# Optimization experiments

Hardware: AMD Instinct MI355X
Metric: run time of the kernel (lower is better)

The kernel has to match this reference:

```python
import jax, jax.numpy as jnp
import numpy as np

N_NODES = 50000
N_EDGES = 1_600_000
NUM_GRAPHS = 64
F_NODE = 32
F_EDGE = 16
H = 64
L = 3
BN_EPS = 1e-5


def setup_inputs() -> dict:
    key = jax.random.key(0)
    ks = jax.random.split(key, 20)
    x = jax.random.normal(ks[0], (N_NODES, F_NODE), jnp.float32)
    edge_attr = jax.random.normal(ks[1], (N_EDGES, F_EDGE), jnp.float32)
    edge_index = jax.random.randint(ks[2], (2, N_EDGES), 0, N_NODES, dtype=jnp.int64)
    batch = jnp.sort(jax.random.randint(ks[3], (N_NODES,), 0, NUM_GRAPHS, dtype=jnp.int64))

    def lin(k, fan_in, shape):
        return jax.random.normal(k, shape, jnp.float32) * (1.0 / np.sqrt(fan_in))

    node_W = lin(ks[4], F_NODE, (F_NODE, H));  node_b = jnp.zeros((H,), jnp.float32)
    edge_W = lin(ks[5], F_EDGE, (F_EDGE, H));  edge_b = jnp.zeros((H,), jnp.float32)
    # GINE per-layer MLP: Linear(H, 2H) -> ReLU -> Linear(2H, H)
    W1s = lin(ks[6], H, (L, H, 2 * H));   b1s = jnp.zeros((L, 2 * H), jnp.float32)
    W2s = lin(ks[7], 2 * H, (L, 2 * H, H)); b2s = jnp.zeros((L, H), jnp.float32)
    gammas = jnp.ones((L, H), jnp.float32)
    betas = jnp.zeros((L, H), jnp.float32)
    lin_W = lin(ks[8], H, (H, 1));  lin_b = jnp.zeros((1,), jnp.float32)
    return {
        "x": x, "edge_attr": edge_attr, "edge_index": edge_index, "batch": batch,
        "node_W": node_W, "node_b": node_b, "edge_W": edge_W, "edge_b": edge_b,
        "W1s": W1s, "b1s": b1s, "W2s": W2s, "b2s": b2s,
        "gammas": gammas, "betas": betas, "lin_W": lin_W, "lin_b": lin_b,
    }


def reference(x, edge_attr, edge_index, batch, node_W, node_b, edge_W, edge_b,
              W1s, b1s, W2s, b2s, gammas, betas, lin_W, lin_b):
    # node / edge embeddings
    h = x @ node_W + node_b                  # [N, H]
    e = edge_attr @ edge_W + edge_b          # [E, H]
    src, dst = edge_index[0], edge_index[1]
    for l in range(L):
        # GINEConv (eps=0): m_ij = relu(x_j + e_ij), aggregate sum at target
        m = jax.nn.relu(h[src] + e)                                  # [E, H]
        agg = jax.ops.segment_sum(m, dst, num_segments=N_NODES)     # [N, H]
        z = h + agg
        z = jax.nn.relu(z @ W1s[l] + b1s[l]) @ W2s[l] + b2s[l]       # GINE MLP
        # BatchNorm (training-mode batch stats, biased variance) + ReLU
        mu = jnp.mean(z, axis=0)
        var = jnp.var(z, axis=0)
        h = jax.nn.relu(gammas[l] * (z - mu) * jax.lax.rsqrt(var + BN_EPS) + betas[l])
    # global mean pool per graph
    counts = jax.ops.segment_sum(jnp.ones((N_NODES,), h.dtype), batch, num_segments=NUM_GRAPHS)
    gsum = jax.ops.segment_sum(h, batch, num_segments=NUM_GRAPHS)   # [G, H]
    graph_x = gsum / jnp.maximum(counts, 1.0)[:, None]
    return graph_x @ lin_W + lin_b                                   # [G, 1]
```

## Files before the change

kernel.cpp:

```cpp
#include <hip/hip_runtime.h>

#define NN 50000
#define NE 1600000
#define NG 64
#define HD 64
#define BN_EPS 1e-5f
#define NTILES ((NN + 31) / 32)

typedef unsigned short ushort_t;
typedef unsigned int uint_t;
typedef __attribute__((ext_vector_type(8))) short bf16x8;
typedef __attribute__((ext_vector_type(4))) float f32x4;

__device__ __forceinline__ float b2f(ushort_t u) {
  union { uint_t i; float f; } v; v.i = ((uint_t)u) << 16; return v.f;
}
__device__ __forceinline__ ushort_t f2b(float f) {
  union { float f; uint_t i; } v; v.f = f;
  uint_t x = v.i;
  return (ushort_t)((x + 0x7fffu + ((x >> 16) & 1u)) >> 16);
}
__device__ __forceinline__ uint_t packsplit(float f) {
  ushort_t hi = f2b(f);
  float r = f - b2f(hi);
  ushort_t lo = f2b(r);
  return (uint_t)hi | ((uint_t)lo << 16);
}
__device__ __forceinline__ float LDF(const void* p, int i, int isb) {
  return isb ? b2f(((const ushort_t*)p)[i]) : ((const float*)p)[i];
}
__device__ __forceinline__ int LDI(const void* p, int i, int is64) {
  return is64 ? ((const int*)p)[2 * i] : ((const int*)p)[i];
}
__device__ __forceinline__ int clampi(int v, int hi) {
  return (v < 0) ? 0 : (v >= hi ? hi - 1 : v);
}

__global__ void detect_k(const uint_t* __restrict__ xw, const uint_t* __restrict__ ew,
                         int* __restrict__ flags) {
  int t = threadIdx.x;
  uint_t w = xw[t];
  uint_t b = (w >> 8) & 0x7fu;
  unsigned long long m1 = __ballot(b >= 0x3au && b <= 0x42u);
  unsigned long long m2 = __ballot(ew[2 * t + 1] == 0u);
  if (t == 0) {
    flags[0] = (__popcll(m1) >= 32) ? 1 : 0;
    flags[1] = (__popcll(m2) >= 56) ? 1 : 0;
  }
}

__global__ void __launch_bounds__(256) node_embed(
    const void* __restrict__ x, const void* __restrict__ W,
    const void* __restrict__ b, float* __restrict__ h, const int* __restrict__ flags) {
  __shared__ float xs[64 * 32];
  int isb = flags[0];
  int t = threadIdx.x;
  int base = blockIdx.x * 64;
  int nodes = NN - base; if (nodes > 64) nodes = 64;
  int idx = t * 8;
  if (idx < nodes * 32) {
    if (isb) {
      const uint4* p = (const uint4*)((const ushort_t*)x + base * 32);
      uint4 u = p[t];
      ushort_t* pu = (ushort_t*)&u;
      #pragma unroll
      for (int q = 0; q < 8; q++) xs[idx + q] = b2f(pu[q]);
    } else {
      const float4* p = (const float4*)((const float*)x + base * 32);
      float4 a = p[2 * t], d = p[2 * t + 1];
      xs[idx + 0] = a.x; xs[idx + 1] = a.y; xs[idx + 2] = a.z; xs[idx + 3] = a.w;
      xs[idx + 4] = d.x; xs[idx + 5] = d.y; xs[idx + 6] = d.z; xs[idx + 7] = d.w;
    }
  }
  int c = t & 63, s0 = t >> 6;
  float w[32];
  #pragma unroll
  for (int k = 0; k < 32; k++) w[k] = LDF(W, k * 64 + c, isb);
  float bc = LDF(b, c, isb);
  __syncthreads();
  #pragma unroll 4
  for (int i = 0; i < 16; i++) {
    int slot = s0 * 16 + i;
    int node = base + slot;
    if (node < NN) {
      float acc = bc;
      #pragma unroll
      for (int k = 0; k < 32; k++) acc += xs[slot * 32 + k] * w[k];
      h[node * 64 + c] = acc;
    }
  }
}

__global__ void __launch_bounds__(256) hist_k(
    const void* __restrict__ eidx, int* __restrict__ hist, const int* __restrict__ flags) {
  int is64 = flags[1];
  int e = blockIdx.x * 256 + threadIdx.x;
  if (e >= NE) return;
  int d = clampi(LDI(eidx, NE + e, is64), NN);
  atomicAdd(&hist[d], 1);
}

__global__ void __launch_bounds__(1024) scan_k(
    const int* __restrict__ hist, int* __restrict__ offs) {
  __shared__ int buf[1024];
  int t = threadIdx.x;
  int beg = t * 49, end = beg + 49; if (end > NN) end = NN; if (beg > NN) beg = NN;
  int s = 0;
  for (int i = beg; i < end; i++) s += hist[i];
  buf[t] = s;
  __syncthreads();
  for (int d = 1; d < 1024; d <<= 1) {
    int x = (t >= d) ? buf[t - d] : 0;
    __syncthreads();
    buf[t] += x;
    __syncthreads();
  }
  int run = buf[t] - s;
  for (int i = beg; i < end; i++) { int hv = hist[i]; offs[i] = run; run += hv; }
  if (t == 1023) offs[NN] = run;
}

__global__ void __launch_bounds__(256) scatter_k(
    const void* __restrict__ eidx, int* __restrict__ cursor,
    int* __restrict__ perm, int* __restrict__ psrc, int* __restrict__ pdst,
    const int* __restrict__ flags) {
  int is64 = flags[1];
  int e = blockIdx.x * 256 + threadIdx.x;
  if (e >= NE) return;
  int d = clampi(LDI(eidx, NE + e, is64), NN);
  int s = clampi(LDI(eidx, e, is64), NN);
  int pos = atomicAdd(&cursor[d], 1);
  perm[pos] = e;
  psrc[pos] = s;
  pdst[pos] = d;
}

__global__ void __launch_bounds__(256) edge_sorted(
    const void* __restrict__ eattr, const int* __restrict__ perm,
    const int* __restrict__ psrc, const int* __restrict__ pdst,
    const void* __restrict__ eW, const void* __restrict__ eb,
    const float* __restrict__ h, float* __restrict__ agg, const int* __restrict__ flags) {
  __shared__ float ea[64 * 16];
  __shared__ int ss[64], sd[64];
  int isb = flags[0];
  int t = threadIdx.x;
  int base = blockIdx.x * 64;
  if (t < 64) ss[t] = psrc[base + t];
  else if (t < 128) sd[t - 64] = pdst[base + t - 64];
  {
    int slot = t >> 2, q = t & 3;
    int pe = perm[base + slot];
    if (isb) {
      const uint2* p = (const uint2*)((const ushort_t*)eattr + (size_t)pe * 16 + q * 4);
      uint2 u = *p;
      ea[slot * 16 + q * 4 + 0] = b2f((ushort_t)(u.x & 0xffffu));
      ea[slot * 16 + q * 4 + 1] = b2f((ushort_t)(u.x >> 16));
      ea[slot * 16 + q * 4 + 2] = b2f((ushort_t)(u.y & 0xffffu));
      ea[slot * 16 + q * 4 + 3] = b2f((ushort_t)(u.y >> 16));
    } else {
      const float4* p = (const float4*)((const float*)eattr + (size_t)pe * 16 + q * 4);
      float4 v = *p;
      ea[slot * 16 + q * 4 + 0] = v.x;
      ea[slot * 16 + q * 4 + 1] = v.y;
      ea[slot * 16 + q * 4 + 2] = v.z;
      ea[slot * 16 + q * 4 + 3] = v.w;
    }
  }
  int c = t & 63, s0 = t >> 6;
  float w[16];
  #pragma unroll
  for (int k = 0; k < 16; k++) w[k] = LDF(eW, k * 64 + c, isb);
  float bc = LDF(eb, c, isb);
  __syncthreads();
  float acc = 0.f;
  int cur = -1;
  for (int i = 0; i < 16; i++) {
    int slot = s0 * 16 + i;
    int sn = ss[slot], dn = sd[slot];
    float e = bc;
    #pragma unroll
    for (int k = 0; k < 16; k++) e += ea[slot * 16 + k] * w[k];
    float m = h[sn * 64 + c] + e;
    m = m > 0.f ? m : 0.f;
    if (dn != cur) {
      if (cur >= 0) atomicAdd(&agg[cur * 64 + c], acc);
      cur = dn; acc = 0.f;
    }
    acc += m;
  }
  if (cur >= 0) atomicAdd(&agg[cur * 64 + c], acc);
}

__global__ void __launch_bounds__(256) prep_w(
    const void* __restrict__ W1s, const void* __restrict__ W2s,
    uint4* __restrict__ wpk, const int* __restrict__ flags) {
  int l = blockIdx.x, t = threadIdx.x, isb = flags[0];
  uint4* w1hi = wpk + (size_t)l * 4096;
  uint4* w1lo = w1hi + 1024;
  uint4* w2hi = w1hi + 2048;
  uint4* w2lo = w1hi + 3072;
  union U8 { ushort_t s[8]; uint4 u; };
  for (int o = t; o < 1024; o += 256) {
    int lane = o & 63, f = (o >> 6) & 7, hh = o >> 9;
    int q = lane >> 4, m = lane & 15;
    {
      int kc = f >> 2, i = f & 3;
      U8 hi, lo;
      #pragma unroll
      for (int j = 0; j < 8; j++) {
        int idx = l * 8192 + (kc * 32 + q * 8 + j) * 128 + (hh * 4 + i) * 16 + m;
        float wf = LDF(W1s, idx, isb);
        ushort_t hb = f2b(wf);
        hi.s[j] = hb;
        lo.s[j] = f2b(wf - b2f(hb));
      }
      w1hi[o] = hi.u;
      w1lo[o] = lo.u;
    }
    {
      int kc = f >> 1, i = f & 1;
      U8 hi, lo;
      #pragma unroll
      for (int j = 0; j < 8; j++) {
        int idx = l * 8192 + (kc * 32 + q * 8 + j) * 64 + (hh * 2 + i) * 16 + m;
        float wf = LDF(W2s, idx, isb);
        ushort_t hb = f2b(wf);
        hi.s[j] = hb;
        lo.s[j] = f2b(wf - b2f(hb));
      }
      w2hi[o] = hi.u;
      w2lo[o] = lo.u;
    }
  }
}

__global__ void __launch_bounds__(256) mlp_mfma(
    const float* __restrict__ h, const float* agg,
    const uint4* __restrict__ wpk, const void* __restrict__ b1s,
    const void* __restrict__ b2s,
    float* z2out, float* __restrict__ bnsum, const int* __restrict__ flags, int layer) {
  __shared__ uint_t zs[32 * 65];
  __shared__ uint_t a1s[32 * 129];
  int isb = flags[0];
  int t = threadIdx.x;
  int w = t >> 6, lane = t & 63, q = lane >> 4, m = lane & 15;
  int mt = w & 1;
  int hh = w >> 1;
  int ng1 = hh * 4;
  int ng2 = hh * 2;
  int b1off = layer * 128, b2off = layer * 64;
  const uint4* w1hi = wpk + (size_t)layer * 4096;
  const uint4* w1lo = w1hi + 1024;
  const uint4* w2hi = w1hi + 2048;
  const uint4* w2lo = w1hi + 3072;

  union FR { uint4 u; bf16x8 v; };
  FR w1f[4][2], w2f[2][4];
  #pragma unroll
  for (int kc = 0; kc < 2; kc++)
    #pragma unroll
    for (int i = 0; i < 4; i++)
      w1f[i][kc].u = w1hi[(hh * 8 + kc * 4 + i) * 64 + lane];
  #pragma unroll
  for (int kc = 0; kc < 4; kc++)
    #pragma unroll
    for (int i = 0; i < 2; i++)
      w2f[i][kc].u = w2hi[(hh * 8 + kc * 2 + i) * 64 + lane];

  float b1v[4], b2v[2];
  #pragma unroll
  for (int i = 0; i < 4; i++) b1v[i] = LDF(b1s, b1off + (ng1 + i) * 16 + m, isb);
  #pragma unroll
  for (int i = 0; i < 2; i++) b2v[i] = LDF(b2s, b2off + (ng2 + i) * 16 + m, isb);

  int srow = t >> 3, scol = (t & 7) * 8;
  float ps[2] = {0.f, 0.f}, pq[2] = {0.f, 0.f};

  for (int tile = blockIdx.x; tile < NTILES; tile += gridDim.x) {
    int base = tile * 32;
    __syncthreads();
    {
      int gr = base + srow;
      if (gr < NN) {
        const float4* hp = (const float4*)(h + (size_t)gr * 64 + scol);
        const float4* ap = (const float4*)(agg + (size_t)gr * 64 + scol);
        float4 h0 = hp[0], h1 = hp[1], a0 = ap[0], a1 = ap[1];
        zs[srow * 65 + scol + 0] = packsplit(h0.x + a0.x);
        zs[srow * 65 + scol + 1] = packsplit(h0.y + a0.y);
        zs[srow * 65 + scol + 2] = packsplit(h0.z + a0.z);
        zs[srow * 65 + scol + 3] = packsplit(h0.w + a0.w);
        zs[srow * 65 + scol + 4] = packsplit(h1.x + a1.x);
        zs[srow * 65 + scol + 5] = packsplit(h1.y + a1.y);
        zs[srow * 65 + scol + 6] = packsplit(h1.z + a1.z);
        zs[srow * 65 + scol + 7] = packsplit(h1.w + a1.w);
      } else {
        #pragma unroll
        for (int jj = 0; jj < 8; jj++) zs[srow * 65 + scol + jj] = 0;
      }
    }
    __syncthreads();
    f32x4 acc1[4];
    #pragma unroll
    for (int i = 0; i < 4; i++) acc1[i] = (f32x4){0.f, 0.f, 0.f, 0.f};
    #pragma unroll
    for (int kc = 0; kc < 2; kc++) {
      int ab = (mt * 16 + m) * 65 + kc * 32 + q * 8;
      bf16x8 ahi, alo;
      #pragma unroll
      for (int j = 0; j < 8; j++) {
        uint_t u = zs[ab + j];
        ahi[j] = (short)(u & 0xffffu);
        alo[j] = (short)(u >> 16);
      }
      #pragma unroll
      for (int i = 0; i < 4; i++) {
        acc1[i] = __builtin_amdgcn_mfma_f32_16x16x32_bf16(ahi, w1f[i][kc].v, acc1[i], 0, 0, 0);
        acc1[i] = __builtin_amdgcn_mfma_f32_16x16x32_bf16(alo, w1f[i][kc].v, acc1[i], 0, 0, 0);
        if (!isb) {
          FR bl;
          bl.u = w1lo[(hh * 8 + kc * 4 + i) * 64 + lane];
          acc1[i] = __builtin_amdgcn_mfma_f32_16x16x32_bf16(ahi, bl.v, acc1[i], 0, 0, 0);
        }
      }
    }
    #pragma unroll
    for (int i = 0; i < 4; i++) {
      #pragma unroll
      for (int r = 0; r < 4; r++) {
        float v = acc1[i][r] + b1v[i];
        v = v > 0.f ? v : 0.f;
        a1s[(mt * 16 + q * 4 + r) * 129 + (ng1 + i) * 16 + m] = packsplit(v);
      }
    }
    __syncthreads();
    f32x4 acc2[2];
    #pragma unroll
    for (int i = 0; i < 2; i++) acc2[i] = (f32x4){0.f, 0.f, 0.f, 0.f};
    #pragma unroll
    for (int kc = 0; kc < 4; kc++) {
      int ab = (mt * 16 + m) * 129 + kc * 32 + q * 8;
      bf16x8 ahi, alo;
      #pragma unroll
      for (int j = 0; j < 8; j++) {
        uint_t u = a1s[ab + j];
        ahi[j] = (short)(u & 0xffffu);
        alo[j] = (short)(u >> 16);
      }
      #pragma unroll
      for (int i = 0; i < 2; i++) {
        acc2[i] = __builtin_amdgcn_mfma_f32_16x16x32_bf16(ahi, w2f[i][kc].v, acc2[i], 0, 0, 0);
        acc2[i] = __builtin_amdgcn_mfma_f32_16x16x32_bf16(alo, w2f[i][kc].v, acc2[i], 0, 0, 0);
        if (!isb) {
          FR bl;
          bl.u = w2lo[(hh * 8 + kc * 2 + i) * 64 + lane];
          acc2[i] = __builtin_amdgcn_mfma_f32_16x16x32_bf16(ahi, bl.v, acc2[i], 0, 0, 0);
        }
      }
    }
    #pragma unroll
    for (int i = 0; i < 2; i++) {
      int col = (ng2 + i) * 16 + m;
      #pragma unroll
      for (int r = 0; r < 4; r++) {
        int gr = base + mt * 16 + q * 4 + r;
        if (gr < NN) {
          float v = acc2[i][r] + b2v[i];
          z2out[(size_t)gr * 64 + col] = v;
          ps[i] += v; pq[i] += v * v;
        }
      }
    }
  }
  __syncthreads();
  float* red = (float*)zs;
  if (t < 128) red[t] = 0.f;
  __syncthreads();
  #pragma unroll
  for (int i = 0; i < 2; i++) {
    int col = (ng2 + i) * 16 + m;
    atomicAdd(&red[col], ps[i]);
    atomicAdd(&red[64 + col], pq[i]);
  }
  __syncthreads();
  if (t < 128) atomicAdd(&bnsum[t], red[t]);
}

__global__ void bn_fin(const float* __restrict__ bnsum, const void* __restrict__ gammas,
                       const void* __restrict__ betas, float* __restrict__ scsh,
                       const int* __restrict__ flags, int layer) {
  int c = threadIdx.x;
  int isb = flags[0];
  float inv_n = 1.0f / (float)NN;
  float mu = bnsum[c] * inv_n;
  float var = bnsum[64 + c] * inv_n - mu * mu;
  var = var > 0.f ? var : 0.f;
  float sc = LDF(gammas, layer * 64 + c, isb) * rsqrtf(var + BN_EPS);
  scsh[c] = sc;
  scsh[64 + c] = LDF(betas, layer * 64 + c, isb) - mu * sc;
}

__global__ void __launch_bounds__(256) bn_apply(
    const float* __restrict__ z2, const float* __restrict__ scsh, float* __restrict__ h) {
  int t = blockIdx.x * 256 + threadIdx.x;
  if (t < NN * 16) {
    float4 z = ((const float4*)z2)[t];
    int c4 = t & 15;
    float4 sc = ((const float4*)scsh)[c4];
    float4 sh = ((const float4*)(scsh + 64))[c4];
    float4 r;
    r.x = fmaxf(z.x * sc.x + sh.x, 0.f);
    r.y = fmaxf(z.y * sc.y + sh.y, 0.f);
    r.z = fmaxf(z.z * sc.z + sh.z, 0.f);
    r.w = fmaxf(z.w * sc.w + sh.w, 0.f);
    ((float4*)h)[t] = r;
  }
}

__global__ void __launch_bounds__(256) find_bounds(
    const void* __restrict__ batch, int* __restrict__ bounds, const int* __restrict__ flags) {
  int is64 = flags[1];
  int i = blockIdx.x * 256 + threadIdx.x;
  if (i >= NN) return;
  int cur = clampi(LDI(batch, i, is64), NG);
  if (i == 0) {
    for (int g = 0; g <= cur; g++) bounds[g] = 0;
  } else {
    int prev = clampi(LDI(batch, i - 1, is64), NG);
    for (int g = prev + 1; g <= cur; g++) bounds[g] = i;
  }
  if (i == NN - 1) {
    for (int g = cur + 1; g <= NG; g++) bounds[g] = NN;
  }
}

__global__ void __launch_bounds__(256) pool_final(
    const float* __restrict__ h, const int* __restrict__ bounds,
    const void* __restrict__ linW, const void* __restrict__ linB,
    float* __restrict__ out, const int* __restrict__ flags) {
  __shared__ float red[4][64];
  int isb = flags[0];
  int g = blockIdx.x;
  int t = threadIdx.x, c = t & 63, w = t >> 6;
  int s = bounds[g], e = bounds[g + 1];
  float acc = 0.f;
  for (int i = s + w; i < e; i += 4) acc += h[i * 64 + c];
  red[w][c] = acc;
  __syncthreads();
  if (t < 64) {
    float v = red[0][c] + red[1][c] + red[2][c] + red[3][c];
    float cnt = (float)(e - s); if (cnt < 1.f) cnt = 1.f;
    v = (v / cnt) * LDF(linW, c, isb);
    #pragma unroll
    for (int m = 32; m >= 1; m >>= 1) v += __shfl_xor(v, m, 64);
    if (c == 0) out[g] = v + LDF(linB, 0, isb);
  }
}

extern "C" void kernel_launch(void* const* d_in, const int* in_sizes, int n_in,
                              void* d_out, int out_size, void* d_ws, size_t ws_size,
                              hipStream_t stream) {
  const void* x     = d_in[0];
  const void* eattr = d_in[1];
  const void* eidx  = d_in[2];
  const void* batch = d_in[3];
  const void* nodeW = d_in[4];
  const void* nodeB = d_in[5];
  const void* edgeW = d_in[6];
  const void* edgeB = d_in[7];
  const void* W1s   = d_in[8];
  const void* b1s   = d_in[9];
  const void* W2s   = d_in[10];
  const void* b2s   = d_in[11];
  const void* gam   = d_in[12];
  const void* bet   = d_in[13];
  const void* linW  = d_in[14];
  const void* linB  = d_in[15];
  float* out = (float*)d_out;

  int*   flags  = (int*)d_ws;
  float* h      = (float*)d_ws + 16;
  float* agg    = h + (size_t)NN * HD;
  float* bnsum  = agg + (size_t)NN * HD;
  float* scsh   = bnsum + 128;
  int*   bounds = (int*)(scsh + 128);
  int*   offs   = bounds + 80;
  int*   cursor = offs + (NN + 1);
  int*   perm   = cursor + (NN + 1);
  int*   psrc   = perm + NE;
  int*   pdst   = psrc + NE;

  size_t base_words = 16ull + 2ull * NN * HD + 128 + 128 + 80;
  size_t sort_words = base_words + 2ull * (NN + 1) + 3ull * NE;
  size_t wpk_words_start = (sort_words + 3ull) & ~3ull;
  size_t wpk_words = 3ull * 4096 * 4;
  size_t needed = (wpk_words_start + wpk_words) * 4ull;
  if (ws_size < needed) return;
  uint4* wpk = (uint4*)((float*)d_ws + wpk_words_start);
  float* z2sep = (float*)d_ws + wpk_words_start + wpk_words;
  float* z2 = (ws_size >= (wpk_words_start + wpk_words + (size_t)NN * HD) * 4ull)
                  ? z2sep : agg;

  detect_k<<<1, 64, 0, stream>>>((const uint_t*)x, (const uint_t*)eidx, flags);
  prep_w<<<3, 256, 0, stream>>>(W1s, W2s, wpk, flags);
  node_embed<<<(NN + 63) / 64, 256, 0, stream>>>(x, nodeW, nodeB, h, flags);

  hipMemsetAsync(offs, 0, (NN + 1) * sizeof(int), stream);
  hist_k<<<NE / 256, 256, 0, stream>>>(eidx, offs, flags);
  scan_k<<<1, 1024, 0, stream>>>(offs, cursor);
  scatter_k<<<NE / 256, 256, 0, stream>>>(eidx, cursor, perm, psrc, pdst, flags);

  for (int l = 0; l < 3; l++) {
    hipMemsetAsync(agg, 0, (size_t)NN * HD * sizeof(float), stream);
    edge_sorted<<<NE / 64, 256, 0, stream>>>(eattr, perm, psrc, pdst, edgeW, edgeB, h, agg, flags);
    hipMemsetAsync(bnsum, 0, 128 * sizeof(float), stream);
    mlp_mfma<<<784, 256, 0, stream>>>(h, agg, wpk, b1s, b2s, z2, bnsum, flags, l);
    bn_fin<<<1, 64, 0, stream>>>(bnsum, gam, bet, scsh, flags, l);
    bn_apply<<<3125, 256, 0, stream>>>(z2, scsh, h);
  }
  find_bounds<<<(NN + 255) / 256, 256, 0, stream>>>(batch, bounds, flags);
  pool_final<<<NG, 256, 0, stream>>>(h, bounds, linW, linB, out, flags);
}
```

Measured before the change: 961.6 us.

## Pre-permute edge attributes into bf16 split tiles and compute edge embedding with MFMA

Adds a one-time kernel that gathers edge attributes in destination-sorted order and stores them as packed bf16 hi/lo fragments laid out per 16-edge tile. Each layer's edge kernel then computes the edge embedding with split-bf16 MFMA instructions instead of a scalar 16-term dot product per channel. This removes the random perm gather of edge_attr and the per-layer scalar FMAs, which are repeated three times. The cost is a large extra workspace and one extra pass, and the path falls back to the old kernel when the workspace is too small.

```diff
diff --git a/kernel.cpp b/kernel.cpp
--- a/kernel.cpp
+++ b/kernel.cpp
@@ -133,6 +133,104 @@
   perm[pos] = e;
   psrc[pos] = s;
   pdst[pos] = d;
+}
+
+__global__ void __launch_bounds__(256) pack_eattr(
+    const void* __restrict__ eattr, const int* __restrict__ perm,
+    ushort_t* __restrict__ phi, ushort_t* __restrict__ plo,
+    const int* __restrict__ flags) {
+  int isb = flags[0];
+  int pos = blockIdx.x * 256 + threadIdx.x;
+  if (pos >= NE) return;
+  int e = perm[pos];
+  int tile = pos >> 4, r = pos & 15;
+  union U8 { ushort_t s[8]; uint4 u; };
+  if (isb) {
+    const uint4* p = (const uint4*)((const ushort_t*)eattr + (size_t)e * 16);
+    uint4 h0 = p[0], h1 = p[1];
+    ((uint4*)phi)[tile * 32 + r] = h0;
+    ((uint4*)phi)[tile * 32 + 16 + r] = h1;
+  } else {
+    const float4* p = (const float4*)((const float*)eattr + (size_t)e * 16);
+    U8 hi[2], lo[2];
+    #pragma unroll
+    for (int q = 0; q < 4; q++) {
+      float4 v = p[q];
+      float vv[4] = {v.x, v.y, v.z, v.w};
+      #pragma unroll
+      for (int j = 0; j < 4; j++) {
+        int idx = q * 4 + j;
+        ushort_t hb = f2b(vv[j]);
+        hi[idx >> 3].s[idx & 7] = hb;
+        lo[idx >> 3].s[idx & 7] = f2b(vv[j] - b2f(hb));
+      }
+    }
+    ((uint4*)phi)[tile * 32 + r] = hi[0].u;
+    ((uint4*)phi)[tile * 32 + 16 + r] = hi[1].u;
+    ((uint4*)plo)[tile * 32 + r] = lo[0].u;
+    ((uint4*)plo)[tile * 32 + 16 + r] = lo[1].u;
+  }
+}
+
+__global__ void __launch_bounds__(256) edge_mfma(
+    const ushort_t* __restrict__ phi, const ushort_t* __restrict__ plo,
+    const int* __restrict__ psrc, const int* __restrict__ pdst,
+    const uint4* __restrict__ wfrag, const float* __restrict__ h,
+    float* __restrict__ agg, const int* __restrict__ flags) {
+  __shared__ float es[64 * 65];
+  __shared__ int ss[64], sd[64];
+  int isb = flags[0];
+  int t = threadIdx.x;
+  int base = blockIdx.x * 64;
+  if (t < 64) ss[t] = psrc[base + t];
+  else if (t < 128) sd[t - 64] = pdst[base + t - 64];
+  int w = t >> 6, lane = t & 63, kg = lane >> 4, cr = lane & 15;
+  int tile = blockIdx.x * 4 + w;
+  union FR { uint4 u; bf16x8 v; };
+  FR ahi, alo;
+  ahi.u = make_uint4(0u, 0u, 0u, 0u);
+  alo.u = ahi.u;
+  if (kg < 2) {
+    ahi.u = ((const uint4*)phi)[tile * 32 + kg * 16 + cr];
+    if (!isb) alo.u = ((const uint4*)plo)[tile * 32 + kg * 16 + cr];
+  }
+  f32x4 acc[4];
+  #pragma unroll
+  for (int nt = 0; nt < 4; nt++) acc[nt] = (f32x4){0.f, 0.f, 0.f, 0.f};
+  #pragma unroll
+  for (int nt = 0; nt < 4; nt++) {
+    FR bh; bh.u = wfrag[nt * 64 + lane];
+    acc[nt] = __builtin_amdgcn_mfma_f32_16x16x32_bf16(ahi.v, bh.v, acc[nt], 0, 0, 0);
+    if (!isb) {
+      FR bl; bl.u = wfrag[256 + nt * 64 + lane];
+      acc[nt] = __builtin_amdgcn_mfma_f32_16x16x32_bf16(ahi.v, bl.v, acc[nt], 0, 0, 0);
+      acc[nt] = __builtin_amdgcn_mfma_f32_16x16x32_bf16(alo.v, bh.v, acc[nt], 0, 0, 0);
+    }
+  }
+  const float* ebias = (const float*)(wfrag + 512);
+  #pragma unroll
+  for (int nt = 0; nt < 4; nt++) {
+    float bv = ebias[nt * 16 + cr];
+    #pragma unroll
+    for (int r = 0; r < 4; r++)
+      es[(w * 16 + kg * 4 + r) * 65 + nt * 16 + cr] = acc[nt][r] + bv;
+  }
+  __syncthreads();
+  int c = lane, s0 = w;
+  float accr = 0.f;
+  int cur = -1;
+  for (int i = 0; i < 16; i++) {
+    int slot = s0 * 16 + i;
+    int sn = ss[slot], dn = sd[slot];
+    float m = h[(size_t)sn * 64 + c] + es[slot * 65 + c];
+    m = m > 0.f ? m : 0.f;
+    if (dn != cur) {
+      if (cur >= 0) atomicAdd(&agg[cur * 64 + c], accr);
+      cur = dn; accr = 0.f;
+    }
+    accr += m;
+  }
+  if (cur >= 0) atomicAdd(&agg[cur * 64 + c], accr);
 }
 
 __global__ void __launch_bounds__(256) edge_sorted(
@@ -193,13 +291,32 @@
 
 __global__ void __launch_bounds__(256) prep_w(
     const void* __restrict__ W1s, const void* __restrict__ W2s,
+    const void* __restrict__ eW, const void* __restrict__ eB,
     uint4* __restrict__ wpk, const int* __restrict__ flags) {
   int l = blockIdx.x, t = threadIdx.x, isb = flags[0];
+  union U8 { ushort_t s[8]; uint4 u; };
+  if (l == 3) {
+    uint4* wfrag = wpk + 3 * 4096;
+    int nt = t >> 6, lane = t & 63;
+    int col = nt * 16 + (lane & 15);
+    U8 hi, lo;
+    #pragma unroll
+    for (int j = 0; j < 8; j++) {
+      int k = (lane >> 4) * 8 + j;
+      float wf = (k < 16) ? LDF(eW, k * 64 + col, isb) : 0.f;
+      ushort_t hb = f2b(wf);
+      hi.s[j] = hb;
+      lo.s[j] = f2b(wf - b2f(hb));
+    }
+    wfrag[nt * 64 + lane] = hi.u;
+    wfrag[256 + nt * 64 + lane] = lo.u;
+    if (t < 64) ((float*)(wfrag + 512))[t] = LDF(eB, t, isb);
+    return;
+  }
   uint4* w1hi = wpk + (size_t)l * 4096;
   uint4* w1lo = w1hi + 1024;
   uint4* w2hi = w1hi + 2048;
   uint4* w2lo = w1hi + 3072;
-  union U8 { ushort_t s[8]; uint4 u; };
   for (int o = t; o < 1024; o += 256) {
     int lane = o & 63, f = (o >> 6) & 7, hh = o >> 9;
     int q = lane >> 4, m = lane & 15;
@@ -492,26 +609,38 @@
   size_t base_words = 16ull + 2ull * NN * HD + 128 + 128 + 80;
   size_t sort_words = base_words + 2ull * (NN + 1) + 3ull * NE;
   size_t wpk_words_start = (sort_words + 3ull) & ~3ull;
-  size_t wpk_words = 3ull * 4096 * 4;
+  size_t wpk_words = (3ull * 4096 + 528) * 4;
   size_t needed = (wpk_words_start + wpk_words) * 4ull;
   if (ws_size < needed) return;
   uint4* wpk = (uint4*)((float*)d_ws + wpk_words_start);
-  float* z2sep = (float*)d_ws + wpk_words_start + wpk_words;
-  float* z2 = (ws_size >= (wpk_words_start + wpk_words + (size_t)NN * HD) * 4ull)
-                  ? z2sep : agg;
+  uint4* wfrag = wpk + 3ull * 4096;
+  size_t z2_start = wpk_words_start + wpk_words;
+  float* z2sep = (float*)d_ws + z2_start;
+  int have_z2 = ws_size >= (z2_start + (size_t)NN * HD) * 4ull;
+  float* z2 = have_z2 ? z2sep : agg;
+  size_t pat_start = z2_start + (size_t)NN * HD;
+  size_t pat_words = (size_t)NE * 8;
+  int have_pat = have_z2 && (ws_size >= (pat_start + 2ull * pat_words) * 4ull);
+  ushort_t* phi = (ushort_t*)((float*)d_ws + pat_start);
+  ushort_t* plo = (ushort_t*)((float*)d_ws + pat_start + pat_words);
 
   detect_k<<<1, 64, 0, stream>>>((const uint_t*)x, (const uint_t*)eidx, flags);
-  prep_w<<<3, 256, 0, stream>>>(W1s, W2s, wpk, flags);
+  prep_w<<<4, 256, 0, stream>>>(W1s, W2s, edgeW, edgeB, wpk, flags);
   node_embed<<<(NN + 63) / 64, 256, 0, stream>>>(x, nodeW, nodeB, h, flags);
 
   hipMemsetAsync(offs, 0, (NN + 1) * sizeof(int), stream);
   hist_k<<<NE / 256, 256, 0, stream>>>(eidx, offs, flags);
   scan_k<<<1, 1024, 0, stream>>>(offs, cursor);
   scatter_k<<<NE / 256, 256, 0, stream>>>(eidx, cursor, perm, psrc, pdst, flags);
+  if (have_pat)
+    pack_eattr<<<NE / 256, 256, 0, stream>>>(eattr, perm, phi, plo, flags);
 
   for (int l = 0; l < 3; l++) {
     hipMemsetAsync(agg, 0, (size_t)NN * HD * sizeof(float), stream);
-    edge_sorted<<<NE / 64, 256, 0, stream>>>(eattr, perm, psrc, pdst, edgeW, edgeB, h, agg, flags);
+    if (have_pat)
+      edge_mfma<<<NE / 64, 256, 0, stream>>>(phi, plo, psrc, pdst, wfrag, h, agg, flags);
+    else
+      edge_sorted<<<NE / 64, 256, 0, stream>>>(eattr, perm, psrc, pdst, edgeW, edgeB, h, agg, flags);
     hipMemsetAsync(bnsum, 0, 128 * sizeof(float), stream);
     mlp_mfma<<<784, 256, 0, stream>>>(h, agg, wpk, b1s, b2s, z2, bnsum, flags, l);
     bn_fin<<<1, 64, 0, stream>>>(bnsum, gam, bet, scsh, flags, l);
```

Result: slower. 1.081 ms (+12.5%).
